# Kernel tuning notes

Hardware: AMD Instinct MI355X
Metric: run time of the kernel (lower is better)

Reference implementation:

```python
import jax, jax.numpy as jnp
import numpy as np

SIZE = 1024
SIZE_INTERNAL = 4096
B, S = 8, 2048
EPS = 1e-5


def layer_norm(x, g, b):
    mu = jnp.mean(x, axis=-1, keepdims=True)
    var = jnp.mean(jnp.square(x - mu), axis=-1, keepdims=True)
    return (x - mu) * jax.lax.rsqrt(var + EPS) * g + b


def setup_inputs() -> dict:
    key = jax.random.key(0)
    ks = jax.random.split(key, 12)
    s = 0.02
    return {
        "x": jax.random.normal(ks[0], (B, S, SIZE), jnp.float32),
        "Wq": jax.random.normal(ks[1], (SIZE, SIZE), jnp.float32) * s,
        "bq": jnp.zeros((SIZE,), jnp.float32),
        "Wk": jax.random.normal(ks[2], (SIZE, SIZE), jnp.float32) * s,
        "bk": jnp.zeros((SIZE,), jnp.float32),
        "Wv": jax.random.normal(ks[3], (SIZE, SIZE), jnp.float32) * s,
        "bv": jnp.zeros((SIZE,), jnp.float32),
        "W1": jax.random.normal(ks[4], (SIZE, SIZE_INTERNAL), jnp.float32) * s,
        "b1": jnp.zeros((SIZE_INTERNAL,), jnp.float32),
        "W2": jax.random.normal(ks[5], (SIZE_INTERNAL, SIZE), jnp.float32) * s,
        "b2": jnp.zeros((SIZE,), jnp.float32),
        "g1": jnp.ones((SIZE,), jnp.float32),
        "beta1": jnp.zeros((SIZE,), jnp.float32),
        "g2": jnp.ones((SIZE,), jnp.float32),
        "beta2": jnp.zeros((SIZE,), jnp.float32),
    }


def reference(x, Wq, bq, Wk, bk, Wv, bv, W1, b1, W2, b2, g1, beta1, g2, beta2):
    # QKV projections (single-head; bmm on 3D tensors in original)
    q = x @ Wq + bq  # (B,S,d)
    k = x @ Wk + bk
    v = x @ Wv + bv
    scale = 1.0 / jnp.sqrt(jnp.asarray(SIZE, x.dtype))
    scores = jnp.einsum("bqd,bkd->bqk", q, k) * scale  # (B,S,S)
    # decoder=True -> causal mask
    causal = jnp.tril(jnp.ones((S, S), bool))
    scores = jnp.where(causal, scores, jnp.asarray(-jnp.inf, x.dtype))
    attn = jax.nn.softmax(scores, axis=-1)
    attn_out = jnp.einsum("bqk,bkd->bqd", attn, v)
    attn_out = layer_norm(attn_out, g1, beta1)
    h = jax.nn.gelu(attn_out @ W1 + b1, approximate=False)
    out = h @ W2 + b2 + attn_out
    return layer_norm(out, g2, beta2)
```

## Files before the change

### kernel.cpp

```cpp
#include <hip/hip_runtime.h>
#include <cstdint>

#define DEV __device__ __forceinline__

typedef __attribute__((ext_vector_type(8))) short bf16x8;
typedef __attribute__((ext_vector_type(4))) float f32x4;
typedef unsigned short u16;
typedef unsigned int   u32;

DEV u16 f2bf(float f) {
  u32 u = __float_as_uint(f);
  u = (u + 0x7FFFu + ((u >> 16) & 1u)) >> 16;
  return (u16)u;
}
DEV float bf2f(u16 s) { return __uint_as_float(((u32)s) << 16); }

DEV float gelu_f(float x) {
  const float x2 = x * x;
  const float z  = x * fmaf(-0.1029436f, x2, -2.3022082f);
  const float e  = exp2f(z);
  return x * (1.f / (1.f + e));
}

DEV void gload_lds16(const void* g, void* l) {
  typedef __attribute__((address_space(1))) const unsigned int GU;
  typedef __attribute__((address_space(3))) unsigned int LU;
  __builtin_amdgcn_global_load_lds((GU*)(uintptr_t)g, (LU*)(u32)(uintptr_t)l, 16, 0, 0);
}

DEV int swz(int x) { return x ^ (((x >> 7) & 7) << 4); }

#define BATCH_SC 2228224L

template<int MODE>
__global__ __launch_bounds__(256, 4)
void gemm_bt(const u16* __restrict__ A, int lda, long abst,
             const u16* __restrict__ Bt, int ldb, long bbst,
             void* __restrict__ Cv, int ldc, long cbst,
             const float* __restrict__ bias,
             const float* __restrict__ bias2,
             const float* __restrict__ bias3,
             int K, float scale)
{
  const int nt = blockIdx.x, mt = blockIdx.y, bz = blockIdx.z;
  if (MODE == 1 && nt > mt) return;
  const int Keff = (MODE == 2) ? (mt + 1) * 128 : K;

  __shared__ u16 As[128 * 64];
  __shared__ u16 Bs[128 * 64];

  const int tid  = threadIdx.x;
  const int lane = tid & 63;
  const int wv   = tid >> 6;
  const int wr   = wv >> 1, wc = wv & 1;
  const int lrow = lane & 15;
  const int kgrp = lane >> 4;
  const int m0 = mt * 128, n0 = nt * 128;

  const int srow = tid >> 3;
  const int scolb = ((tid & 7) * 16) ^ ((srow & 7) << 4);
  const u16* Ag;
  if (MODE == 2) {
    Ag = A + bz * BATCH_SC + (long)(mt * (mt + 1) / 2) * 16384 + srow * 128 + (scolb >> 1);
  } else {
    Ag = A + (long)bz * abst + (long)(m0 + srow) * lda + (scolb >> 1);
  }
  const u16* Bg = Bt + (long)bz * bbst + (long)(n0 + srow) * ldb + (scolb >> 1);
  char* AsW = (char*)As + wv * 1024;
  char* BsW = (char*)Bs + wv * 1024;

  f32x4 acc[4][4];
#pragma unroll
  for (int mi = 0; mi < 4; ++mi)
#pragma unroll
    for (int ni = 0; ni < 4; ++ni)
#pragma unroll
      for (int e = 0; e < 4; ++e) acc[mi][ni][e] = 0.f;

  for (int k0 = 0; k0 < Keff; k0 += 64) {
#pragma unroll
    for (int i = 0; i < 4; ++i) {
      if (MODE == 2)
        gload_lds16(Ag + (long)(k0 >> 7) * 16384 + (k0 & 127) + i * 32 * 128, AsW + i * 4096);
      else
        gload_lds16(Ag + k0 + (long)i * 32 * lda, AsW + i * 4096);
      gload_lds16(Bg + k0 + (long)i * 32 * ldb, BsW + i * 4096);
    }
    __syncthreads();
#pragma unroll
    for (int kk = 0; kk < 2; ++kk) {
      const int kofb = (kk * 64 + kgrp * 16) ^ ((lrow & 7) << 4);
      bf16x8 af[4], bfr[4];
#pragma unroll
      for (int mi = 0; mi < 4; ++mi)
        af[mi] = *(const bf16x8*)((const char*)As + (wr * 64 + mi * 16 + lrow) * 128 + kofb);
#pragma unroll
      for (int ni = 0; ni < 4; ++ni)
        bfr[ni] = *(const bf16x8*)((const char*)Bs + (wc * 64 + ni * 16 + lrow) * 128 + kofb);
#pragma unroll
      for (int mi = 0; mi < 4; ++mi)
#pragma unroll
        for (int ni = 0; ni < 4; ++ni)
          acc[mi][ni] = __builtin_amdgcn_mfma_f32_16x16x32_bf16(af[mi], bfr[ni], acc[mi][ni], 0, 0, 0);
    }
    __syncthreads();
  }

#pragma unroll
  for (int mi = 0; mi < 4; ++mi) {
#pragma unroll
    for (int ni = 0; ni < 4; ++ni) {
#pragma unroll
      for (int e = 0; e < 4; ++e) {
        const int rr = wr * 64 + mi * 16 + kgrp * 4 + e;
        const int cc = wc * 64 + ni * 16 + lrow;
        const int gr = m0 + rr, gc = n0 + cc;
        const float v = acc[mi][ni][e];
        if (MODE == 0) {
          const float bval = gc < 1024 ? bias[gc]
                              : (gc < 2048 ? bias2[gc & 1023] : bias3[gc & 1023]);
          ((u16*)Cv)[(long)(gc >> 10) * 16777216 + (long)gr * 1024 + (gc & 1023)]
              = f2bf(v + bval);
        } else if (MODE == 1) {
          ((u16*)Cv)[bz * BATCH_SC + (long)(mt * (mt + 1) / 2 + nt) * 16384 + rr * 128 + cc]
              = f2bf(v * scale);
        } else if (MODE == 2) {
          ((u16*)Cv)[(long)bz * cbst + (long)gr * ldc + gc] = f2bf(v);
        } else if (MODE == 3) {
          ((u16*)Cv)[(long)gr * ldc + gc] = f2bf(gelu_f(v + bias[gc]));
        }
      }
    }
  }
}

template<int PASS>
__global__ __launch_bounds__(512, 2)
void gemm256_p8_ffn2(const u16* __restrict__ A, int lda,
                     const u16* __restrict__ Bt, int ldb,
                     void* __restrict__ Cv, int ldc,
                     const float* __restrict__ bias,
                     const u16* __restrict__ resid,
                     int K, int NNT)
{
  __shared__ char smem[131072];
  const int tid  = threadIdx.x;
  const int lane = tid & 63;
  const int wv   = tid >> 6;
  const int wm   = wv >> 2, wn = wv & 3;
  const int lrow = lane & 15;
  const int kgrp = lane >> 4;

  const int nwg = gridDim.x;
  const int q0 = nwg >> 3, r = nwg & 7, xc = blockIdx.x & 7, pos = blockIdx.x >> 3;
  const int s = (xc < r ? xc * (q0 + 1) : r * (q0 + 1) + (xc - r) * q0) + pos;
  const int mt = s / NNT, nt = s % NNT;
  const int m0 = mt * 256, n0 = nt * 256;

  auto stageA = [&](int ktile, int dslot, int h) {
    int k0 = ktile << 6; const int kmax = K - 64; if (k0 > kmax) k0 = kmax;
#pragma unroll
    for (int j = 0; j < 2; ++j) {
      const int o = j * 8192 + tid * 16;
      const int l = swz(o);
      gload_lds16(A + (long)(m0 + h * 128 + (l >> 7)) * lda + k0 + ((l & 127) >> 1),
                  smem + dslot * 65536 + h * 16384 + o);
    }
  };
  auto stageB = [&](int ktile, int dslot, int h) {
    int k0 = ktile << 6; const int kmax = K - 64; if (k0 > kmax) k0 = kmax;
#pragma unroll
    for (int j = 0; j < 2; ++j) {
      const int o = j * 8192 + tid * 16;
      const int l = swz(o);
      gload_lds16(Bt + (long)(n0 + h * 128 + (l >> 7)) * ldb + k0 + ((l & 127) >> 1),
                  smem + dslot * 65536 + 32768 + h * 16384 + o);
    }
  };
  auto rdfrag = [&](int bofs, int row, int ks) -> bf16x8 {
    const int p = swz(row * 128 + ks * 64 + kgrp * 16);
    return *(const bf16x8*)(smem + bofs + p);
  };

  f32x4 acc[8][4];
#pragma unroll
  for (int mi = 0; mi < 8; ++mi)
#pragma unroll
    for (int ni = 0; ni < 4; ++ni)
#pragma unroll
      for (int e = 0; e < 4; ++e) acc[mi][ni][e] = 0.f;

  stageA(0, 0, 0); stageA(0, 0, 1); stageB(0, 0, 0); stageB(0, 0, 1);
  stageB(1, 1, 0); stageB(1, 1, 1);
  asm volatile("s_waitcnt vmcnt(4)" ::: "memory");
  __builtin_amdgcn_s_barrier();

  const int NI = K >> 7;
  bf16x8 bfrag[4][2], afrag[2][2];
  for (int i = 0; i < NI; ++i) {
    const int kp = 2 * i;
#pragma unroll
    for (int d = 0; d < 2; ++d) {
#pragma unroll
      for (int mq = 0; mq < 4; ++mq) {
        const int ph = d * 4 + mq;
        if (mq == 0) {
#pragma unroll
          for (int ni = 0; ni < 4; ++ni)
#pragma unroll
            for (int ks = 0; ks < 2; ++ks)
              bfrag[ni][ks] = rdfrag(d * 65536 + 32768, wn * 64 + ni * 16 + lrow, ks);
        }
#pragma unroll
        for (int mi2 = 0; mi2 < 2; ++mi2)
#pragma unroll
          for (int ks = 0; ks < 2; ++ks)
            afrag[mi2][ks] = rdfrag(d * 65536, wm * 128 + (2 * mq + mi2) * 16 + lrow, ks);
        switch (ph) {
          case 0: stageA(kp + 1, 1, 0); break;
          case 1: stageA(kp + 1, 1, 1); break;
          case 2: stageB(kp + 2, 0, 0); break;
          case 3: stageB(kp + 2, 0, 1); break;
          case 4: stageA(kp + 2, 0, 0); break;
          case 5: stageA(kp + 2, 0, 1); break;
          case 6: stageB(kp + 3, 1, 0); break;
          case 7: stageB(kp + 3, 1, 1); break;
        }
        __builtin_amdgcn_s_barrier();
        asm volatile("s_waitcnt lgkmcnt(0)" ::: "memory");
        __builtin_amdgcn_s_setprio(1);
#pragma unroll
        for (int mi2 = 0; mi2 < 2; ++mi2)
#pragma unroll
          for (int ni = 0; ni < 4; ++ni)
#pragma unroll
            for (int ks = 0; ks < 2; ++ks)
              acc[2 * mq + mi2][ni] = __builtin_amdgcn_mfma_f32_16x16x32_bf16(
                  afrag[mi2][ks], bfrag[ni][ks], acc[2 * mq + mi2][ni], 0, 0, 0);
        __builtin_amdgcn_s_setprio(0);
        if (mq == 3) asm volatile("s_waitcnt vmcnt(4)" ::: "memory");
        __builtin_amdgcn_s_barrier();
      }
    }
  }

#pragma unroll
  for (int mi = 0; mi < 8; ++mi) {
#pragma unroll
    for (int ni = 0; ni < 4; ++ni) {
      const int gc = n0 + wn * 64 + ni * 16 + lrow;
#pragma unroll
      for (int e = 0; e < 4; ++e) {
        const int gr = m0 + wm * 128 + mi * 16 + kgrp * 4 + e;
        if (PASS == 0) {
          ((float*)Cv)[(long)gr * ldc + gc] = acc[mi][ni][e];
        } else if (PASS == 1) {
          float* o = &((float*)Cv)[(long)gr * ldc + gc];
          *o = *o + acc[mi][ni][e] + bias[gc] + bf2f(resid[(long)gr * 1024 + gc]);
        } else {
          ((u16*)Cv)[(long)gr * ldc + gc]
              = f2bf(acc[mi][ni][e] + bias[gc] + bf2f(resid[(long)gr * 1024 + gc]));
        }
      }
    }
  }
}

__global__ __launch_bounds__(256)
void prep_weights(const float* __restrict__ Wq, const float* __restrict__ Wk,
                  const float* __restrict__ Wv, const float* __restrict__ W1,
                  const float* __restrict__ W2,
                  u16* __restrict__ wqkvT, u16* __restrict__ w1T, u16* __restrict__ w2T)
{
  const int idx = blockIdx.x;
  const float* in; u16* out; int R, C, cx0, ry0;
  if (idx < 3072) {
    in = (idx < 1024) ? Wq : (idx < 2048 ? Wk : Wv);
    out = wqkvT + (long)(idx >> 10) * 1048576;
    const int i = idx & 1023; cx0 = (i & 31) * 32; ry0 = (i >> 5) * 32; R = 1024; C = 1024;
  } else if (idx < 7168) {
    const int i = idx - 3072; in = W1; out = w1T; R = 1024; C = 4096;
    cx0 = (i & 127) * 32; ry0 = (i >> 7) * 32;
  } else {
    const int i = idx - 7168; in = W2; out = w2T; R = 4096; C = 1024;
    cx0 = (i & 31) * 32; ry0 = (i >> 5) * 32;
  }
  __shared__ float t[32][33];
  const int tx = threadIdx.x & 31, ty = threadIdx.x >> 5;
#pragma unroll
  for (int i = 0; i < 32; i += 8)
    t[ty + i][tx] = in[(long)(ry0 + ty + i) * C + (cx0 + tx)];
  __syncthreads();
#pragma unroll
  for (int i = 0; i < 32; i += 8)
    out[(long)(cx0 + ty + i) * R + (ry0 + tx)] = f2bf(t[tx][ty + i]);
}

__global__ __launch_bounds__(256)
void transpose_v(const u16* __restrict__ inv, u16* __restrict__ out,
                 int R, int C, long ibst, long obst)
{
  __shared__ float t[32][33];
  const int bz = blockIdx.z;
  const int c0 = blockIdx.x * 32, r0 = blockIdx.y * 32;
  const int tx = threadIdx.x & 31, ty = threadIdx.x >> 5;
#pragma unroll
  for (int i = 0; i < 32; i += 8) {
    const long idx = (long)bz * ibst + (long)(r0 + ty + i) * C + (c0 + tx);
    t[ty + i][tx] = bf2f(inv[idx]);
  }
  __syncthreads();
#pragma unroll
  for (int i = 0; i < 32; i += 8)
    out[(long)bz * obst + (long)(c0 + ty + i) * R + (r0 + tx)] = f2bf(t[tx][ty + i]);
}

__global__ __launch_bounds__(256)
void cvt_f32_to_bf16(const float* __restrict__ in, u16* __restrict__ out, long n)
{
  const long idx = ((long)blockIdx.x * 256 + threadIdx.x) * 4;
  if (idx >= n) return;
  const float4 v = *(const float4*)(in + idx);
  ushort4 o;
  o.x = f2bf(v.x); o.y = f2bf(v.y); o.z = f2bf(v.z); o.w = f2bf(v.w);
  *(ushort4*)(out + idx) = o;
}

__global__ __launch_bounds__(256)
void softmax_packed(u16* __restrict__ sc)
{
  const int rowid = blockIdx.x;
  const int b = rowid >> 11, i = rowid & 2047;
  const int mtt = i >> 7, rr = i & 127;
  u16* base = sc + (long)b * BATCH_SC + (long)(mtt * (mtt + 1) / 2) * 16384 + (long)rr * 128;
  const int t = threadIdx.x;
  const int lane = t & 63, wv = t >> 6;
  const int c   = t >> 4;
  const int off = (t & 15) * 8;
  const bool act = (c <= mtt);
  const int lim = (c < mtt) ? 8 : (c == mtt ? (rr - off + 1) : 0);
  u16* p = base + (long)c * 16384 + off;

  bf16x8 vv = {};
  if (act) vv = *(const bf16x8*)p;
  float vals[8];
  float m = -1e30f;
#pragma unroll
  for (int e = 0; e < 8; ++e) {
    vals[e] = (e < lim) ? bf2f((u16)vv[e]) : -1e30f;
    m = fmaxf(m, vals[e]);
  }
#pragma unroll
  for (int o = 1; o < 64; o <<= 1) m = fmaxf(m, __shfl_xor(m, o));
  __shared__ float rm[4], rsm[4];
  if (lane == 0) rm[wv] = m;
  __syncthreads();
  m = fmaxf(fmaxf(rm[0], rm[1]), fmaxf(rm[2], rm[3]));
  float pv[8];
  float ssum = 0.f;
#pragma unroll
  for (int e = 0; e < 8; ++e) { pv[e] = __expf(vals[e] - m); ssum += pv[e]; }
#pragma unroll
  for (int o = 1; o < 64; o <<= 1) ssum += __shfl_xor(ssum, o);
  if (lane == 0) rsm[wv] = ssum;
  __syncthreads();
  ssum = rsm[0] + rsm[1] + rsm[2] + rsm[3];
  const float inv = 1.f / ssum;
  if (act) {
    bf16x8 o;
#pragma unroll
    for (int e = 0; e < 8; ++e) o[e] = (short)f2bf(pv[e] * inv);
    *(bf16x8*)p = o;
  }
}

template<int INBF, int OUTBF>
__global__ __launch_bounds__(256)
void layernorm_k(const void* __restrict__ in, const float* __restrict__ gam,
                 const float* __restrict__ bet, void* __restrict__ outv)
{
  const long row = blockIdx.x;
  const int t = threadIdx.x;
  const int lane = t & 63, wv = t >> 6;
  float v0, v1, v2, v3;
  if (INBF) {
    const ushort4 u = ((const ushort4*)in)[row * 256 + t];
    v0 = bf2f(u.x); v1 = bf2f(u.y); v2 = bf2f(u.z); v3 = bf2f(u.w);
  } else {
    const float4 v = ((const float4*)in)[row * 256 + t];
    v0 = v.x; v1 = v.y; v2 = v.z; v3 = v.w;
  }
  float s = v0 + v1 + v2 + v3;
  float q = v0 * v0 + v1 * v1 + v2 * v2 + v3 * v3;
#pragma unroll
  for (int o = 1; o < 64; o <<= 1) { s += __shfl_xor(s, o); q += __shfl_xor(q, o); }
  __shared__ float rs[4], rq[4];
  if (lane == 0) { rs[wv] = s; rq[wv] = q; }
  __syncthreads();
  s = rs[0] + rs[1] + rs[2] + rs[3];
  q = rq[0] + rq[1] + rq[2] + rq[3];
  const float mean = s * (1.f / 1024.f);
  const float var  = q * (1.f / 1024.f) - mean * mean;
  const float rstd = rsqrtf(var + 1e-5f);
  const float4 g4 = ((const float4*)gam)[t];
  const float4 b4 = ((const float4*)bet)[t];
  const float o0 = (v0 - mean) * rstd * g4.x + b4.x;
  const float o1 = (v1 - mean) * rstd * g4.y + b4.y;
  const float o2 = (v2 - mean) * rstd * g4.z + b4.z;
  const float o3 = (v3 - mean) * rstd * g4.w + b4.w;
  if (OUTBF) {
    ushort4 o; o.x = f2bf(o0); o.y = f2bf(o1); o.z = f2bf(o2); o.w = f2bf(o3);
    ((ushort4*)outv)[row * 256 + t] = o;
  } else {
    ((float4*)outv)[row * 256 + t] = make_float4(o0, o1, o2, o3);
  }
}

extern "C" void kernel_launch(void* const* d_in, const int* in_sizes, int n_in,
                              void* d_out, int out_size, void* d_ws, size_t ws_size,
                              hipStream_t stream)
{
  const float* x   = (const float*)d_in[0];
  const float* Wq  = (const float*)d_in[1];
  const float* bq  = (const float*)d_in[2];
  const float* Wk  = (const float*)d_in[3];
  const float* bk  = (const float*)d_in[4];
  const float* Wv  = (const float*)d_in[5];
  const float* bv  = (const float*)d_in[6];
  const float* W1  = (const float*)d_in[7];
  const float* b1  = (const float*)d_in[8];
  const float* W2  = (const float*)d_in[9];
  const float* b2  = (const float*)d_in[10];
  const float* g1  = (const float*)d_in[11];
  const float* be1 = (const float*)d_in[12];
  const float* g2  = (const float*)d_in[13];
  const float* be2 = (const float*)d_in[14];

  char* ws = (char*)d_ws;
  u16*   wqkvT = (u16*)(ws);
  u16*   w1T   = (u16*)(ws + 6291456);
  u16*   w2T   = (u16*)(ws + 14680064);
  u16*   xb    = (u16*)(ws + 23068672);
  u16*   vt    = xb;
  u16*   f2out = xb;
  u16*   qkv   = (u16*)(ws + 56623104);
  u16*   qbuf  = qkv;
  u16*   kbuf  = qkv + 16777216;
  u16*   vbuf  = qkv + 33554432;
  u16*   ln1   = qbuf;
  u16*   pvout = kbuf;
  u16*   sc    = (u16*)(ws + 123731968);
  u16*   hbuf  = kbuf;
  const bool big = (ws_size >= 224395264ULL);

  const dim3 B256(256);

  cvt_f32_to_bf16<<<dim3(16384), B256, 0, stream>>>(x, xb, 16777216L);

  prep_weights<<<dim3(11264), B256, 0, stream>>>(Wq, Wk, Wv, W1, W2, wqkvT, w1T, w2T);

  gemm_bt<0><<<dim3(24, 128), B256, 0, stream>>>(xb, 1024, 0, wqkvT, 1024, 0, qkv, 1024, 0,
                                                 bq, bk, bv, 1024, 1.f);

  transpose_v<<<dim3(32, 64, 8), B256, 0, stream>>>(vbuf, vt, 2048, 1024, 2097152, 2097152);

  gemm_bt<1><<<dim3(16, 16, 8), B256, 0, stream>>>(qbuf, 1024, 2097152, kbuf, 1024, 2097152,
                                                   sc, 0, 0, nullptr, nullptr, nullptr,
                                                   1024, 0.03125f);

  softmax_packed<<<dim3(16384), B256, 0, stream>>>(sc);

  gemm_bt<2><<<dim3(8, 16, 8), B256, 0, stream>>>(sc, 0, 0, vt, 2048, 2097152,
                                                  pvout, 1024, 2097152, nullptr, nullptr,
                                                  nullptr, 0, 1.f);

  layernorm_k<1, 1><<<dim3(16384), B256, 0, stream>>>(pvout, g1, be1, ln1);

  if (big) {
    gemm_bt<3><<<dim3(32, 128), B256, 0, stream>>>(ln1, 1024, 0, w1T, 1024, 0, hbuf, 4096, 0,
                                                   b1, nullptr, nullptr, 1024, 1.f);
    gemm256_p8_ffn2<2><<<dim3(256), dim3(512), 0, stream>>>(hbuf, 4096, w2T, 4096,
                                                            f2out, 1024, b2, ln1, 4096, 4);
    layernorm_k<1, 0><<<dim3(16384), B256, 0, stream>>>(f2out, g2, be2, d_out);
  } else {
    for (int j = 0; j < 2; ++j) {
      const u16* w1h = w1T + (long)j * 2048 * 1024;
      gemm_bt<3><<<dim3(16, 128), B256, 0, stream>>>(ln1, 1024, 0, w1h, 1024, 0, hbuf, 2048, 0,
                                                     b1 + j * 2048, nullptr, nullptr,
                                                     1024, 1.f);
      if (j == 0)
        gemm256_p8_ffn2<0><<<dim3(256), dim3(512), 0, stream>>>(hbuf, 2048, w2T, 4096,
                                                                d_out, 1024,
                                                                nullptr, nullptr, 2048, 4);
      else
        gemm256_p8_ffn2<1><<<dim3(256), dim3(512), 0, stream>>>(hbuf, 2048, w2T + 2048, 4096,
                                                                d_out, 1024,
                                                                b2, ln1, 2048, 4);
    }
    layernorm_k<0, 0><<<dim3(16384), B256, 0, stream>>>(d_out, g2, be2, d_out);
  }
}
```

Measured before the change: 611.6 us.

## Merge input conversion with weight prep, remap GEMM tiles per XCD, raise occupancy

```diff
diff --git a/kernel.cpp b/kernel.cpp
--- a/kernel.cpp
+++ b/kernel.cpp
@@ -33,7 +33,7 @@
 #define BATCH_SC 2228224L
 
 template<int MODE>
-__global__ __launch_bounds__(256, 4)
+__global__ __launch_bounds__(256, 5)
 void gemm_bt(const u16* __restrict__ A, int lda, long abst,
              const u16* __restrict__ Bt, int ldb, long bbst,
              void* __restrict__ Cv, int ldc, long cbst,
@@ -42,7 +42,19 @@
              const float* __restrict__ bias3,
              int K, float scale)
 {
-  const int nt = blockIdx.x, mt = blockIdx.y, bz = blockIdx.z;
+  int nt, mt;
+  const int bz = blockIdx.z;
+  if (MODE == 0 || MODE == 3) {
+    const int nwg = gridDim.x * gridDim.y;
+    const int bid = blockIdx.y * gridDim.x + blockIdx.x;
+    const int q0 = nwg >> 3, xc = bid & 7, pos = bid >> 3;
+    const int s = xc * q0 + pos;
+    nt = s % gridDim.x;
+    mt = s / gridDim.x;
+  } else {
+    nt = blockIdx.x;
+    mt = blockIdx.y;
+  }
   if (MODE == 1 && nt > mt) return;
   const int Keff = (MODE == 2) ? (mt + 1) * 128 : K;
 
@@ -267,12 +279,22 @@
 }
 
 __global__ __launch_bounds__(256)
-void prep_weights(const float* __restrict__ Wq, const float* __restrict__ Wk,
-                  const float* __restrict__ Wv, const float* __restrict__ W1,
-                  const float* __restrict__ W2,
-                  u16* __restrict__ wqkvT, u16* __restrict__ w1T, u16* __restrict__ w2T)
-{
-  const int idx = blockIdx.x;
+void prep_all(const float* __restrict__ x, u16* __restrict__ xb,
+              const float* __restrict__ Wq, const float* __restrict__ Wk,
+              const float* __restrict__ Wv, const float* __restrict__ W1,
+              const float* __restrict__ W2,
+              u16* __restrict__ wqkvT, u16* __restrict__ w1T, u16* __restrict__ w2T)
+{
+  const int bidx = blockIdx.x;
+  if (bidx < 16384) {
+    const long idx = ((long)bidx * 256 + threadIdx.x) * 4;
+    const float4 v = *(const float4*)(x + idx);
+    ushort4 o;
+    o.x = f2bf(v.x); o.y = f2bf(v.y); o.z = f2bf(v.z); o.w = f2bf(v.w);
+    *(ushort4*)(xb + idx) = o;
+    return;
+  }
+  const int idx = bidx - 16384;
   const float* in; u16* out; int R, C, cx0, ry0;
   if (idx < 3072) {
     in = (idx < 1024) ? Wq : (idx < 2048 ? Wk : Wv);
@@ -313,17 +335,6 @@
 #pragma unroll
   for (int i = 0; i < 32; i += 8)
     out[(long)bz * obst + (long)(c0 + ty + i) * R + (r0 + tx)] = f2bf(t[tx][ty + i]);
-}
-
-__global__ __launch_bounds__(256)
-void cvt_f32_to_bf16(const float* __restrict__ in, u16* __restrict__ out, long n)
-{
-  const long idx = ((long)blockIdx.x * 256 + threadIdx.x) * 4;
-  if (idx >= n) return;
-  const float4 v = *(const float4*)(in + idx);
-  ushort4 o;
-  o.x = f2bf(v.x); o.y = f2bf(v.y); o.z = f2bf(v.z); o.w = f2bf(v.w);
-  *(ushort4*)(out + idx) = o;
 }
 
 __global__ __launch_bounds__(256)
@@ -455,9 +466,7 @@
 
   const dim3 B256(256);
 
-  cvt_f32_to_bf16<<<dim3(16384), B256, 0, stream>>>(x, xb, 16777216L);
-
-  prep_weights<<<dim3(11264), B256, 0, stream>>>(Wq, Wk, Wv, W1, W2, wqkvT, w1T, w2T);
+  prep_all<<<dim3(27648), B256, 0, stream>>>(x, xb, Wq, Wk, Wv, W1, W2, wqkvT, w1T, w2T);
 
   gemm_bt<0><<<dim3(24, 128), B256, 0, stream>>>(xb, 1024, 0, wqkvT, 1024, 0, qkv, 1024, 0,
                                                  bq, bk, bv, 1024, 1.f);
```

Measured after the change: 1.233 ms. 2.02x slower.
